# Kernel tuning notes

Measured on AMD Instinct MI355X. Metric: run time of the kernel, lower is better.

Reference implementation:

```python
import jax, jax.numpy as jnp
import numpy as np

B, T, I, H, L = 32768, 30, 4, 64, 32


def _lstm_layer(x, Wih, Whh, bih, bhh):
    """PyTorch-semantics single-layer LSTM, batch_first. Returns (outputs [B,T,H], h_T [B,H])."""
    # Precompute input contribution for all timesteps: [B, T, 4H]
    xg = jnp.einsum('bti,gi->btg', x, Wih) + bih + bhh
    Hh = Whh.shape[1]
    h0 = jnp.zeros((x.shape[0], Hh), x.dtype)

    def step(carry, xg_t):
        h, c = carry
        g = xg_t + h @ Whh.T  # [B, 4H]
        i, f, gg, o = jnp.split(g, 4, axis=-1)  # PyTorch gate order i,f,g,o
        c = jax.nn.sigmoid(f) * c + jax.nn.sigmoid(i) * jnp.tanh(gg)
        h = jax.nn.sigmoid(o) * jnp.tanh(c)
        return (h, c), h

    (hT, _), hs = jax.lax.scan(step, (h0, h0), jnp.swapaxes(xg, 0, 1))
    return jnp.swapaxes(hs, 0, 1), hT


def setup_inputs() -> dict:
    key = jax.random.key(0)
    ks = jax.random.split(key, 20)
    s = 0.1  # weight scale for numerical stability
    inp = {
        'x': jax.random.normal(ks[0], (B, T, I), jnp.float32),
        'enc1_Wih': s * jax.random.normal(ks[1], (4 * H, I), jnp.float32),
        'enc1_Whh': s * jax.random.normal(ks[2], (4 * H, H), jnp.float32),
        'enc1_bih': s * jax.random.normal(ks[3], (4 * H,), jnp.float32),
        'enc1_bhh': s * jax.random.normal(ks[4], (4 * H,), jnp.float32),
        'enc2_Wih': s * jax.random.normal(ks[5], (4 * L, H), jnp.float32),
        'enc2_Whh': s * jax.random.normal(ks[6], (4 * L, L), jnp.float32),
        'enc2_bih': s * jax.random.normal(ks[7], (4 * L,), jnp.float32),
        'enc2_bhh': s * jax.random.normal(ks[8], (4 * L,), jnp.float32),
        'dec1_Wih': s * jax.random.normal(ks[9], (4 * H, L), jnp.float32),
        'dec1_Whh': s * jax.random.normal(ks[10], (4 * H, H), jnp.float32),
        'dec1_bih': s * jax.random.normal(ks[11], (4 * H,), jnp.float32),
        'dec1_bhh': s * jax.random.normal(ks[12], (4 * H,), jnp.float32),
        'dec2_Wih': s * jax.random.normal(ks[13], (4 * I, H), jnp.float32),
        'dec2_Whh': s * jax.random.normal(ks[14], (4 * I, I), jnp.float32),
        'dec2_bih': s * jax.random.normal(ks[15], (4 * I,), jnp.float32),
        'dec2_bhh': s * jax.random.normal(ks[16], (4 * I,), jnp.float32),
    }
    return inp


def reference(x, enc1_Wih, enc1_Whh, enc1_bih, enc1_bhh,
              enc2_Wih, enc2_Whh, enc2_bih, enc2_bhh,
              dec1_Wih, dec1_Whh, dec1_bih, dec1_bhh,
              dec2_Wih, dec2_Whh, dec2_bih, dec2_bhh):
    seq_len = x.shape[1]
    out, _ = _lstm_layer(x, enc1_Wih, enc1_Whh, enc1_bih, enc1_bhh)
    out, h = _lstm_layer(out, enc2_Wih, enc2_Whh, enc2_bih, enc2_bhh)
    latent = jnp.repeat(h[:, None, :], seq_len, axis=1)  # [B, T, L]
    out, _ = _lstm_layer(latent, dec1_Wih, dec1_Whh, dec1_bih, dec1_bhh)
    out, _ = _lstm_layer(out, dec2_Wih, dec2_Whh, dec2_bih, dec2_bhh)
    return out
```

## Files before the change

kernel.cpp:

```cpp
#include <hip/hip_runtime.h>
#include <stdint.h>


typedef unsigned short u16;
typedef unsigned int u32;
typedef __attribute__((ext_vector_type(8))) short bf16x8;
typedef __attribute__((ext_vector_type(4))) float f32x4;
typedef __attribute__((ext_vector_type(4))) u32 u32x4;
typedef __attribute__((ext_vector_type(2))) u32 u32x2;

#define BATCH 32768
#define TT 30
#define IN 4
#define WAVES 8
#define BLOCKT (WAVES * 64)
#define MB 16
#define BPB (WAVES * MB)

#define LOG2E 1.4426950408889634f
#define LOG2E2 2.8853900817779268f

#define O_WHH1 0
#define O_W1C  8192
#define O_WIH2 9216
#define O_WHH2 13312
#define O_WHH3 0
#define O_WIH3 8192
#define O_WIH4 12288
#define O_W4HHF 12800
#define O_B1F 15360
#define O_B2F 15616
#define O_B3F 15744
#define O_B4F 16000
#define O_BUFS 16016
#define PBUF 1088
#define SMEM_WORDS (O_BUFS + WAVES * PBUF)
#define SMEM_BYTES (SMEM_WORDS * 4)

#define WB() __builtin_amdgcn_wave_barrier()
#define MFMA(a, b, c) __builtin_amdgcn_mfma_f32_16x16x32_bf16((a), (b), (c), 0, 0, 0)

__device__ __forceinline__ u16 f2bf(float f) {
    u32 u = __float_as_uint(f);
    u += 0x7fffu + ((u >> 16) & 1u);
    return (u16)(u >> 16);
}
__device__ __forceinline__ float bf2f(u16 v) { return __uint_as_float(((u32)v) << 16); }

__device__ __forceinline__ u32 cvtpk2(float a, float b) {
    u32 d;
    asm("v_cvt_pk_bf16_f32 %0, %1, %2" : "=v"(d) : "v"(a), "v"(b));
    return d;
}

__device__ __forceinline__ float unitH(float yi, float yf, float yg, float yo, float& c) {
    const float ei = __builtin_amdgcn_exp2f(-yi);
    const float ef = __builtin_amdgcn_exp2f(-yf);
    const float eg = __builtin_amdgcn_exp2f(yg);
    const float eo = __builtin_amdgcn_exp2f(-yo);
    const float Z = (1.f + ei) * (1.f + eg);
    const float X = 1.f + ef;
    const float num = fmaf(eg - 1.f, X, c * Z);
    c = num * __builtin_amdgcn_rcpf(X * Z);
    const float ec = __builtin_amdgcn_exp2f(c * LOG2E2);
    return (ec - 1.f) * __builtin_amdgcn_rcpf((1.f + eo) * (1.f + ec));
}

template <int KT, int GS>
__device__ __forceinline__ void stageBh(u16* hi, const float* src, int N, int tid) {
    const int K = KT * 32;
    const int total = N * K;
    for (int idx = tid; idx < total; idx += BLOCKT) {
        const int j = idx & 7;
        const int l = (idx >> 3) & 63;
        const int pr = idx >> 9;
        const int kt = pr & (KT - 1);
        const int nt = pr / KT;
        const int n = (nt << 4) | (l & 15);
        const int k = (kt << 5) + ((l >> 4) << 3) + j;
        const float s = (((n >> GS) & 3) == 2) ? LOG2E2 : LOG2E;
        hi[idx] = f2bf(src[n * K + k] * s);
    }
}

__global__ __launch_bounds__(BLOCKT)
__attribute__((amdgpu_waves_per_eu(2)))
void lstm_ae(
    const float* __restrict__ x,
    const float* __restrict__ w1ih, const float* __restrict__ w1hh,
    const float* __restrict__ b1i, const float* __restrict__ b1h,
    const float* __restrict__ w2ih, const float* __restrict__ w2hh,
    const float* __restrict__ b2i, const float* __restrict__ b2h,
    const float* __restrict__ w3ih, const float* __restrict__ w3hh,
    const float* __restrict__ b3i, const float* __restrict__ b3h,
    const float* __restrict__ w4ih, const float* __restrict__ w4hh,
    const float* __restrict__ b4i, const float* __restrict__ b4h,
    float* __restrict__ out) {
    extern __shared__ float smem[];
    float* W = smem;

    const int tid = threadIdx.x;
    const int wave = tid >> 6, lane = tid & 63;
    const int col = lane & 15, quad = lane >> 4;

    float* pb = smem + O_BUFS + wave * PBUF;
    u16* h1b = (u16*)pb;
    u16* h2b = (u16*)(pb + 512);
    float* gbuf = pb + 768;
    float* bufH4 = pb + 1024;

    const int b0w = blockIdx.x * BPB + wave * MB;
    const int hbase = (col << 3) + ((quad & 1) << 2) + ((quad >> 1) << 7);

    stageBh<2, 6>((u16*)(W + O_WHH1), w1hh, 256, tid);
    stageBh<2, 5>((u16*)(W + O_WIH2), w2ih, 128, tid);
    stageBh<1, 5>((u16*)(W + O_WHH2), w2hh, 128, tid);
    {
        u16* C = (u16*)(W + O_W1C);
        for (int idx = tid; idx < 2048; idx += BLOCKT) {
            const int n = idx >> 3, j = idx & 7;
            const float sc = ((n >> 6) == 2) ? LOG2E2 : LOG2E;
            const float w = w1ih[n * 4 + (j & 3)] * sc;
            C[idx] = (j < 4) ? f2bf(w) : f2bf(w - bf2f(f2bf(w)));
        }
    }
    float* b1f = W + O_B1F;
    float* b2f = W + O_B2F;
    float* b3f = W + O_B3F;
    float* b4f = W + O_B4F;
    for (int i = tid; i < 256; i += BLOCKT)
        b1f[i] = (b1i[i] + b1h[i]) * (((i >> 6) == 2) ? LOG2E2 : LOG2E);
    for (int i = tid; i < 128; i += BLOCKT)
        b2f[i] = (b2i[i] + b2h[i]) * (((i >> 5) == 2) ? LOG2E2 : LOG2E);
    for (int i = tid; i < 256; i += BLOCKT)
        b3f[i] = (b3i[i] + b3h[i]) * (((i >> 6) == 2) ? LOG2E2 : LOG2E);
    for (int i = tid; i < 16; i += BLOCKT)
        b4f[i] = (b4i[i] + b4h[i]) * (((i >> 2) == 2) ? LOG2E2 : LOG2E);
    {
        u32* z = (u32*)pb;
        for (int i = lane; i < 768; i += 64) z[i] = 0u;
    }
    __syncthreads();

    const u16* Whh1hi = (const u16*)(W + O_WHH1);
    const u16* Wih2hi = (const u16*)(W + O_WIH2);
    const u16* Whh2hi = (const u16*)(W + O_WHH2);
    const u16* W1cL = (const u16*)(W + O_W1C) + (col << 3) + ((quad == 1) ? 4 : 0);

    float c1[4][4];
    float c2[2][4];
#pragma unroll
    for (int q = 0; q < 4; ++q)
#pragma unroll
        for (int r = 0; r < 4; ++r) c1[q][r] = 0.f;
#pragma unroll
    for (int q = 0; q < 2; ++q)
#pragma unroll
        for (int r = 0; r < 4; ++r) c2[q][r] = 0.f;

    float4 xcur = *reinterpret_cast<const float4*>(x + ((size_t)(b0w + col) * TT + 0) * IN);

    for (int s = 0; s < TT; ++s) {
        const u32 hi01 = cvtpk2(xcur.x, xcur.y);
        const u32 hi23 = cvtpk2(xcur.z, xcur.w);
        const float r0 = xcur.x - __uint_as_float(hi01 << 16);
        const float r1 = xcur.y - __uint_as_float(hi01 & 0xffff0000u);
        const float r2 = xcur.z - __uint_as_float(hi23 << 16);
        const float r3 = xcur.w - __uint_as_float(hi23 & 0xffff0000u);
        const u32 lo01 = cvtpk2(r0, r1);
        const u32 lo23 = cvtpk2(r2, r3);
        u32x4 xv;
        xv.x = (quad <= 1) ? hi01 : 0u;
        xv.y = (quad <= 1) ? hi23 : 0u;
        xv.z = (quad == 0) ? lo01 : 0u;
        xv.w = (quad == 0) ? lo23 : 0u;
        const bf16x8 a1x = __builtin_bit_cast(bf16x8, xv);
        {
            const int tn = (s + 1 < TT) ? s + 1 : s;
            xcur = *reinterpret_cast<const float4*>(x + ((size_t)(b0w + col) * TT + tn) * IN);
        }
        const bf16x8 a1h0 = *reinterpret_cast<const bf16x8*>(h1b + lane * 8);
        const bf16x8 a1h1 = *reinterpret_cast<const bf16x8*>(h1b + (64 + lane) * 8);
#pragma unroll
        for (int q = 0; q < 4; ++q) {
            f32x4 acc[4];
#pragma unroll
            for (int i = 0; i < 4; ++i) {
                const int nt = i * 4 + q;
                const u32x2 wp = *reinterpret_cast<const u32x2*>(W1cL + nt * 128);
                u32x4 afu;
                afu.x = wp.x; afu.y = wp.y; afu.z = wp.x; afu.w = wp.y;
                const bf16x8 af = __builtin_bit_cast(bf16x8, afu);
                const bf16x8 bh0 = *reinterpret_cast<const bf16x8*>(Whh1hi + ((nt * 2 + 0) * 64 + lane) * 8);
                const bf16x8 bh1 = *reinterpret_cast<const bf16x8*>(Whh1hi + ((nt * 2 + 1) * 64 + lane) * 8);
                f32x4 a = *reinterpret_cast<const f32x4*>(b1f + nt * 16 + (quad << 2));
                a = MFMA(af, a1x, a);
                a = MFMA(bh0, a1h0, a);
                a = MFMA(bh1, a1h1, a);
                acc[i] = a;
            }
            const float h0 = unitH(acc[0][0], acc[1][0], acc[2][0], acc[3][0], c1[q][0]);
            const float h1 = unitH(acc[0][1], acc[1][1], acc[2][1], acc[3][1], c1[q][1]);
            const float h2 = unitH(acc[0][2], acc[1][2], acc[2][2], acc[3][2], c1[q][2]);
            const float h3 = unitH(acc[0][3], acc[1][3], acc[2][3], acc[3][3], c1[q][3]);
            u32x2 wv;
            wv.x = cvtpk2(h0, h1);
            wv.y = cvtpk2(h2, h3);
            *reinterpret_cast<u32x2*>(h1b + hbase + ((q >> 1) << 9) + ((q & 1) << 8)) = wv;
        }
        WB();
        const bf16x8 e1h0 = *reinterpret_cast<const bf16x8*>(h1b + lane * 8);
        const bf16x8 e1h1 = *reinterpret_cast<const bf16x8*>(h1b + (64 + lane) * 8);
        const bf16x8 a2h = *reinterpret_cast<const bf16x8*>(h2b + lane * 8);
        f32x4 acc2[8];
#pragma unroll
        for (int nt = 0; nt < 8; ++nt) {
            const bf16x8 bh0 = *reinterpret_cast<const bf16x8*>(Wih2hi + ((nt * 2 + 0) * 64 + lane) * 8);
            const bf16x8 bh1 = *reinterpret_cast<const bf16x8*>(Wih2hi + ((nt * 2 + 1) * 64 + lane) * 8);
            const bf16x8 ch = *reinterpret_cast<const bf16x8*>(Whh2hi + (nt * 64 + lane) * 8);
            f32x4 a = *reinterpret_cast<const f32x4*>(b2f + nt * 16 + (quad << 2));
            a = MFMA(bh0, e1h0, a);
            a = MFMA(bh1, e1h1, a);
            a = MFMA(ch, a2h, a);
            acc2[nt] = a;
        }
        WB();
#pragma unroll
        for (int q = 0; q < 2; ++q) {
            const float h0 = unitH(acc2[q][0], acc2[2 + q][0], acc2[4 + q][0], acc2[6 + q][0], c2[q][0]);
            const float h1 = unitH(acc2[q][1], acc2[2 + q][1], acc2[4 + q][1], acc2[6 + q][1], c2[q][1]);
            const float h2 = unitH(acc2[q][2], acc2[2 + q][2], acc2[4 + q][2], acc2[6 + q][2], c2[q][2]);
            const float h3 = unitH(acc2[q][3], acc2[2 + q][3], acc2[4 + q][3], acc2[6 + q][3], c2[q][3]);
            u32x2 wv;
            wv.x = cvtpk2(h0, h1);
            wv.y = cvtpk2(h2, h3);
            *reinterpret_cast<u32x2*>(h2b + hbase + (q << 8)) = wv;
        }
        WB();
    }

    __syncthreads();
    stageBh<2, 6>((u16*)(W + O_WHH3), w3hh, 256, tid);
    stageBh<1, 6>((u16*)(W + O_WIH3), w3ih, 256, tid);
    stageBh<2, 2>((u16*)(W + O_WIH4), w4ih, 16, tid);
    for (int i = tid; i < 64; i += BLOCKT)
        W[O_W4HHF + i] = w4hh[i] * ((((i >> 4) & 3) == 2) ? LOG2E2 : LOG2E);

    const bf16x8 aLh = *reinterpret_cast<const bf16x8*>(h2b + lane * 8);
    {
        u32* z = (u32*)pb;
        for (int i = lane; i < 512; i += 64) z[i] = 0u;
        bufH4[lane] = 0.f;
    }
    float c3[4][4];
#pragma unroll
    for (int q = 0; q < 4; ++q)
#pragma unroll
        for (int r = 0; r < 4; ++r) c3[q][r] = 0.f;
    float c4 = 0.f;
    const f32x4 bias4v = *reinterpret_cast<const f32x4*>(b4f + (quad << 2));
    const int u4 = lane & 3, mb = lane >> 2;
    __syncthreads();

    const u16* Whh3hi = (const u16*)(W + O_WHH3);
    const u16* Wih3hi = (const u16*)(W + O_WIH3);
    const u16* Wih4hi = (const u16*)(W + O_WIH4);
    const float* W4hhF = W + O_W4HHF;

    for (int s = 0; s < TT; ++s) {
        const bf16x8 a3h0 = *reinterpret_cast<const bf16x8*>(h1b + lane * 8);
        const bf16x8 a3h1 = *reinterpret_cast<const bf16x8*>(h1b + (64 + lane) * 8);
#pragma unroll
        for (int q = 0; q < 4; ++q) {
            f32x4 acc[4];
#pragma unroll
            for (int i = 0; i < 4; ++i) {
                const int nt = i * 4 + q;
                const bf16x8 bL = *reinterpret_cast<const bf16x8*>(Wih3hi + (nt * 64 + lane) * 8);
                const bf16x8 bh0 = *reinterpret_cast<const bf16x8*>(Whh3hi + ((nt * 2 + 0) * 64 + lane) * 8);
                const bf16x8 bh1 = *reinterpret_cast<const bf16x8*>(Whh3hi + ((nt * 2 + 1) * 64 + lane) * 8);
                f32x4 a = *reinterpret_cast<const f32x4*>(b3f + nt * 16 + (quad << 2));
                a = MFMA(bL, aLh, a);
                a = MFMA(bh0, a3h0, a);
                a = MFMA(bh1, a3h1, a);
                acc[i] = a;
            }
            const float h0 = unitH(acc[0][0], acc[1][0], acc[2][0], acc[3][0], c3[q][0]);
            const float h1 = unitH(acc[0][1], acc[1][1], acc[2][1], acc[3][1], c3[q][1]);
            const float h2 = unitH(acc[0][2], acc[1][2], acc[2][2], acc[3][2], c3[q][2]);
            const float h3 = unitH(acc[0][3], acc[1][3], acc[2][3], acc[3][3], c3[q][3]);
            u32x2 wv;
            wv.x = cvtpk2(h0, h1);
            wv.y = cvtpk2(h2, h3);
            *reinterpret_cast<u32x2*>(h1b + hbase + ((q >> 1) << 9) + ((q & 1) << 8)) = wv;
        }
        WB();
        const bf16x8 d3h0 = *reinterpret_cast<const bf16x8*>(h1b + lane * 8);
        const bf16x8 d3h1 = *reinterpret_cast<const bf16x8*>(h1b + (64 + lane) * 8);
        f32x4 acc4 = bias4v;
        {
            const float4 hv = *reinterpret_cast<const float4*>(bufH4 + (col << 2));
#pragma unroll
            for (int r = 0; r < 4; ++r) {
                const float4 w4 = *reinterpret_cast<const float4*>(W4hhF + ((quad * 4 + r) << 2));
                float sa = acc4[r];
                sa = fmaf(w4.x, hv.x, sa);
                sa = fmaf(w4.y, hv.y, sa);
                sa = fmaf(w4.z, hv.z, sa);
                sa = fmaf(w4.w, hv.w, sa);
                acc4[r] = sa;
            }
        }
        {
            const bf16x8 bh0 = *reinterpret_cast<const bf16x8*>(Wih4hi + (0 * 64 + lane) * 8);
            const bf16x8 bh1 = *reinterpret_cast<const bf16x8*>(Wih4hi + (1 * 64 + lane) * 8);
            acc4 = MFMA(bh0, d3h0, acc4);
            acc4 = MFMA(bh1, d3h1, acc4);
        }
        WB();
        *reinterpret_cast<f32x4*>(gbuf + (col << 4) + (quad << 2)) = acc4;
        WB();
        {
            const float yi = gbuf[mb * 16 + u4];
            const float yf = gbuf[mb * 16 + 4 + u4];
            const float yg = gbuf[mb * 16 + 8 + u4];
            const float yo = gbuf[mb * 16 + 12 + u4];
            const float h = unitH(yi, yf, yg, yo, c4);
            out[((size_t)(b0w + mb) * TT + s) * IN + u4] = h;
            bufH4[mb * 4 + u4] = h;
        }
        WB();
    }
}

extern "C" void kernel_launch(void* const* d_in, const int* in_sizes, int n_in,
                              void* d_out, int out_size, void* d_ws, size_t ws_size,
                              hipStream_t stream) {
    (void)in_sizes; (void)n_in; (void)d_ws; (void)ws_size; (void)out_size;
    hipFuncSetAttribute(reinterpret_cast<const void*>(lstm_ae),
                        hipFuncAttributeMaxDynamicSharedMemorySize, SMEM_BYTES);
    const float* xi = (const float*)d_in[0];
    const float* w1ih = (const float*)d_in[1];
    const float* w1hh = (const float*)d_in[2];
    const float* b1i = (const float*)d_in[3];
    const float* b1h = (const float*)d_in[4];
    const float* w2ih = (const float*)d_in[5];
    const float* w2hh = (const float*)d_in[6];
    const float* b2i = (const float*)d_in[7];
    const float* b2h = (const float*)d_in[8];
    const float* w3ih = (const float*)d_in[9];
    const float* w3hh = (const float*)d_in[10];
    const float* b3i = (const float*)d_in[11];
    const float* b3h = (const float*)d_in[12];
    const float* w4ih = (const float*)d_in[13];
    const float* w4hh = (const float*)d_in[14];
    const float* b4i = (const float*)d_in[15];
    const float* b4h = (const float*)d_in[16];
    float* out = (float*)d_out;

    lstm_ae<<<dim3(BATCH / BPB), dim3(BLOCKT), SMEM_BYTES, stream>>>(
        xi, w1ih, w1hh, b1i, b1h, w2ih, w2hh, b2i, b2h,
        w3ih, w3hh, b3i, b3h, w4ih, w4hh, b4i, b4h, out);
}
```

Baseline: 311.3 us.

## Software-pipeline stacked LSTM layers with double-buffered hidden state

Restructures the encoder and decoder time loops so the next step of layer 1 is computed while layer 2 consumes the current step, using a double-buffered h1 in LDS (per-wave buffer grows). This removes several wave barriers per step and exposes more independent MFMA and transcendental work for interleaving. Biases and small dec2 weights are also hoisted into registers, which raises register pressure and may lower occupancy.

```diff
diff --git a/kernel.cpp b/kernel.cpp
--- a/kernel.cpp
+++ b/kernel.cpp
@@ -33,7 +33,7 @@
 #define O_B3F 15744
 #define O_B4F 16000
 #define O_BUFS 16016
-#define PBUF 1088
+#define PBUF 1600
 #define SMEM_WORDS (O_BUFS + WAVES * PBUF)
 #define SMEM_BYTES (SMEM_WORDS * 4)
 
@@ -104,10 +104,10 @@
     const int col = lane & 15, quad = lane >> 4;
 
     float* pb = smem + O_BUFS + wave * PBUF;
-    u16* h1b = (u16*)pb;
-    u16* h2b = (u16*)(pb + 512);
-    float* gbuf = pb + 768;
-    float* bufH4 = pb + 1024;
+    u16* h1d = (u16*)pb;
+    u16* h2b = (u16*)(pb + 1024);
+    float* gbuf = pb + 1280;
+    float* bufH4 = pb + 1536;
 
     const int b0w = blockIdx.x * BPB + wave * MB;
     const int hbase = (col << 3) + ((quad & 1) << 2) + ((quad >> 1) << 7);
@@ -138,7 +138,8 @@
         b4f[i] = (b4i[i] + b4h[i]) * (((i >> 2) == 2) ? LOG2E2 : LOG2E);
     {
         u32* z = (u32*)pb;
-        for (int i = lane; i < 768; i += 64) z[i] = 0u;
+        for (int i = lane; i < 256; i += 64) z[1024 + i] = 0u;
+        bufH4[lane] = 0.f;
     }
     __syncthreads();
 
@@ -147,6 +148,11 @@
     const u16* Whh2hi = (const u16*)(W + O_WHH2);
     const u16* W1cL = (const u16*)(W + O_W1C) + (col << 3) + ((quad == 1) ? 4 : 0);
 
+    f32x4 b2r[8];
+#pragma unroll
+    for (int nt = 0; nt < 8; ++nt)
+        b2r[nt] = *reinterpret_cast<const f32x4*>(b2f + nt * 16 + (quad << 2));
+
     float c1[4][4];
     float c2[2][4];
 #pragma unroll
@@ -160,13 +166,18 @@
 
     float4 xcur = *reinterpret_cast<const float4*>(x + ((size_t)(b0w + col) * TT + 0) * IN);
 
-    for (int s = 0; s < TT; ++s) {
-        const u32 hi01 = cvtpk2(xcur.x, xcur.y);
-        const u32 hi23 = cvtpk2(xcur.z, xcur.w);
-        const float r0 = xcur.x - __uint_as_float(hi01 << 16);
-        const float r1 = xcur.y - __uint_as_float(hi01 & 0xffff0000u);
-        const float r2 = xcur.z - __uint_as_float(hi23 << 16);
-        const float r3 = xcur.w - __uint_as_float(hi23 & 0xffff0000u);
+    auto enc1_step = [&](const bf16x8 ah0, const bf16x8 ah1, u16* hnext, int tnext) {
+        const float4 xc = xcur;
+        {
+            const int tn = (tnext + 1 < TT) ? tnext + 1 : tnext;
+            xcur = *reinterpret_cast<const float4*>(x + ((size_t)(b0w + col) * TT + tn) * IN);
+        }
+        const u32 hi01 = cvtpk2(xc.x, xc.y);
+        const u32 hi23 = cvtpk2(xc.z, xc.w);
+        const float r0 = xc.x - __uint_as_float(hi01 << 16);
+        const float r1 = xc.y - __uint_as_float(hi01 & 0xffff0000u);
+        const float r2 = xc.z - __uint_as_float(hi23 << 16);
+        const float r3 = xc.w - __uint_as_float(hi23 & 0xffff0000u);
         const u32 lo01 = cvtpk2(r0, r1);
         const u32 lo23 = cvtpk2(r2, r3);
         u32x4 xv;
@@ -175,12 +186,6 @@
         xv.z = (quad == 0) ? lo01 : 0u;
         xv.w = (quad == 0) ? lo23 : 0u;
         const bf16x8 a1x = __builtin_bit_cast(bf16x8, xv);
-        {
-            const int tn = (s + 1 < TT) ? s + 1 : s;
-            xcur = *reinterpret_cast<const float4*>(x + ((size_t)(b0w + col) * TT + tn) * IN);
-        }
-        const bf16x8 a1h0 = *reinterpret_cast<const bf16x8*>(h1b + lane * 8);
-        const bf16x8 a1h1 = *reinterpret_cast<const bf16x8*>(h1b + (64 + lane) * 8);
 #pragma unroll
         for (int q = 0; q < 4; ++q) {
             f32x4 acc[4];
@@ -195,8 +200,8 @@
                 const bf16x8 bh1 = *reinterpret_cast<const bf16x8*>(Whh1hi + ((nt * 2 + 1) * 64 + lane) * 8);
                 f32x4 a = *reinterpret_cast<const f32x4*>(b1f + nt * 16 + (quad << 2));
                 a = MFMA(af, a1x, a);
-                a = MFMA(bh0, a1h0, a);
-                a = MFMA(bh1, a1h1, a);
+                a = MFMA(bh0, ah0, a);
+                a = MFMA(bh1, ah1, a);
                 acc[i] = a;
             }
             const float h0 = unitH(acc[0][0], acc[1][0], acc[2][0], acc[3][0], c1[q][0]);
@@ -206,11 +211,18 @@
             u32x2 wv;
             wv.x = cvtpk2(h0, h1);
             wv.y = cvtpk2(h2, h3);
-            *reinterpret_cast<u32x2*>(h1b + hbase + ((q >> 1) << 9) + ((q & 1) << 8)) = wv;
-        }
-        WB();
-        const bf16x8 e1h0 = *reinterpret_cast<const bf16x8*>(h1b + lane * 8);
-        const bf16x8 e1h1 = *reinterpret_cast<const bf16x8*>(h1b + (64 + lane) * 8);
+            *reinterpret_cast<u32x2*>(hnext + hbase + ((q >> 1) << 9) + ((q & 1) << 8)) = wv;
+        }
+    };
+
+    {
+        const bf16x8 z8 = {};
+        enc1_step(z8, z8, h1d, 0);
+    }
+    for (int t = 0; t < TT - 1; ++t) {
+        const u16* hcur = h1d + ((t & 1) << 10);
+        const bf16x8 ah0 = *reinterpret_cast<const bf16x8*>(hcur + lane * 8);
+        const bf16x8 ah1 = *reinterpret_cast<const bf16x8*>(hcur + (64 + lane) * 8);
         const bf16x8 a2h = *reinterpret_cast<const bf16x8*>(h2b + lane * 8);
         f32x4 acc2[8];
 #pragma unroll
@@ -218,13 +230,13 @@
             const bf16x8 bh0 = *reinterpret_cast<const bf16x8*>(Wih2hi + ((nt * 2 + 0) * 64 + lane) * 8);
             const bf16x8 bh1 = *reinterpret_cast<const bf16x8*>(Wih2hi + ((nt * 2 + 1) * 64 + lane) * 8);
             const bf16x8 ch = *reinterpret_cast<const bf16x8*>(Whh2hi + (nt * 64 + lane) * 8);
-            f32x4 a = *reinterpret_cast<const f32x4*>(b2f + nt * 16 + (quad << 2));
-            a = MFMA(bh0, e1h0, a);
-            a = MFMA(bh1, e1h1, a);
+            f32x4 a = b2r[nt];
+            a = MFMA(bh0, ah0, a);
+            a = MFMA(bh1, ah1, a);
             a = MFMA(ch, a2h, a);
             acc2[nt] = a;
         }
-        WB();
+        enc1_step(ah0, ah1, h1d + (((t + 1) & 1) << 10), t + 1);
 #pragma unroll
         for (int q = 0; q < 2; ++q) {
             const float h0 = unitH(acc2[q][0], acc2[2 + q][0], acc2[4 + q][0], acc2[6 + q][0], c2[q][0]);
@@ -236,7 +248,35 @@
             wv.y = cvtpk2(h2, h3);
             *reinterpret_cast<u32x2*>(h2b + hbase + (q << 8)) = wv;
         }
-        WB();
+    }
+    {
+        const u16* hcur = h1d + (((TT - 1) & 1) << 10);
+        const bf16x8 ah0 = *reinterpret_cast<const bf16x8*>(hcur + lane * 8);
+        const bf16x8 ah1 = *reinterpret_cast<const bf16x8*>(hcur + (64 + lane) * 8);
+        const bf16x8 a2h = *reinterpret_cast<const bf16x8*>(h2b + lane * 8);
+        f32x4 acc2[8];
+#pragma unroll
+        for (int nt = 0; nt < 8; ++nt) {
+            const bf16x8 bh0 = *reinterpret_cast<const bf16x8*>(Wih2hi + ((nt * 2 + 0) * 64 + lane) * 8);
+            const bf16x8 bh1 = *reinterpret_cast<const bf16x8*>(Wih2hi + ((nt * 2 + 1) * 64 + lane) * 8);
+            const bf16x8 ch = *reinterpret_cast<const bf16x8*>(Whh2hi + (nt * 64 + lane) * 8);
+            f32x4 a = b2r[nt];
+            a = MFMA(bh0, ah0, a);
+            a = MFMA(bh1, ah1, a);
+            a = MFMA(ch, a2h, a);
+            acc2[nt] = a;
+        }
+#pragma unroll
+        for (int q = 0; q < 2; ++q) {
+            const float h0 = unitH(acc2[q][0], acc2[2 + q][0], acc2[4 + q][0], acc2[6 + q][0], c2[q][0]);
+            const float h1 = unitH(acc2[q][1], acc2[2 + q][1], acc2[4 + q][1], acc2[6 + q][1], c2[q][1]);
+            const float h2 = unitH(acc2[q][2], acc2[2 + q][2], acc2[4 + q][2], acc2[6 + q][2], c2[q][2]);
+            const float h3 = unitH(acc2[q][3], acc2[2 + q][3], acc2[4 + q][3], acc2[6 + q][3], c2[q][3]);
+            u32x2 wv;
+            wv.x = cvtpk2(h0, h1);
+            wv.y = cvtpk2(h2, h3);
+            *reinterpret_cast<u32x2*>(h2b + hbase + (q << 8)) = wv;
+        }
     }
 
     __syncthreads();
@@ -247,29 +287,30 @@
         W[O_W4HHF + i] = w4hh[i] * ((((i >> 4) & 3) == 2) ? LOG2E2 : LOG2E);
 
     const bf16x8 aLh = *reinterpret_cast<const bf16x8*>(h2b + lane * 8);
-    {
-        u32* z = (u32*)pb;
-        for (int i = lane; i < 512; i += 64) z[i] = 0u;
-        bufH4[lane] = 0.f;
-    }
     float c3[4][4];
 #pragma unroll
     for (int q = 0; q < 4; ++q)
 #pragma unroll
         for (int r = 0; r < 4; ++r) c3[q][r] = 0.f;
     float c4 = 0.f;
-    const f32x4 bias4v = *reinterpret_cast<const f32x4*>(b4f + (quad << 2));
     const int u4 = lane & 3, mb = lane >> 2;
     __syncthreads();
 
     const u16* Whh3hi = (const u16*)(W + O_WHH3);
     const u16* Wih3hi = (const u16*)(W + O_WIH3);
-    const u16* Wih4hi = (const u16*)(W + O_WIH4);
-    const float* W4hhF = W + O_W4HHF;
-
-    for (int s = 0; s < TT; ++s) {
-        const bf16x8 a3h0 = *reinterpret_cast<const bf16x8*>(h1b + lane * 8);
-        const bf16x8 a3h1 = *reinterpret_cast<const bf16x8*>(h1b + (64 + lane) * 8);
+    f32x4 b3r[16];
+#pragma unroll
+    for (int nt = 0; nt < 16; ++nt)
+        b3r[nt] = *reinterpret_cast<const f32x4*>(b3f + nt * 16 + (quad << 2));
+    const f32x4 bias4v = *reinterpret_cast<const f32x4*>(b4f + (quad << 2));
+    const bf16x8 w4f0 = *reinterpret_cast<const bf16x8*>((const u16*)(W + O_WIH4) + (0 * 64 + lane) * 8);
+    const bf16x8 w4f1 = *reinterpret_cast<const bf16x8*>((const u16*)(W + O_WIH4) + (1 * 64 + lane) * 8);
+    float4 w4r[4];
+#pragma unroll
+    for (int r = 0; r < 4; ++r)
+        w4r[r] = *reinterpret_cast<const float4*>(W + O_W4HHF + ((quad * 4 + r) << 2));
+
+    auto dec1_step = [&](const bf16x8 ah0, const bf16x8 ah1, u16* hnext) {
 #pragma unroll
         for (int q = 0; q < 4; ++q) {
             f32x4 acc[4];
@@ -279,10 +320,9 @@
                 const bf16x8 bL = *reinterpret_cast<const bf16x8*>(Wih3hi + (nt * 64 + lane) * 8);
                 const bf16x8 bh0 = *reinterpret_cast<const bf16x8*>(Whh3hi + ((nt * 2 + 0) * 64 + lane) * 8);
                 const bf16x8 bh1 = *reinterpret_cast<const bf16x8*>(Whh3hi + ((nt * 2 + 1) * 64 + lane) * 8);
-                f32x4 a = *reinterpret_cast<const f32x4*>(b3f + nt * 16 + (quad << 2));
-                a = MFMA(bL, aLh, a);
-                a = MFMA(bh0, a3h0, a);
-                a = MFMA(bh1, a3h1, a);
+                f32x4 a = MFMA(bL, aLh, b3r[nt]);
+                a = MFMA(bh0, ah0, a);
+                a = MFMA(bh1, ah1, a);
                 acc[i] = a;
             }
             const float h0 = unitH(acc[0][0], acc[1][0], acc[2][0], acc[3][0], c3[q][0]);
@@ -292,31 +332,34 @@
             u32x2 wv;
             wv.x = cvtpk2(h0, h1);
             wv.y = cvtpk2(h2, h3);
-            *reinterpret_cast<u32x2*>(h1b + hbase + ((q >> 1) << 9) + ((q & 1) << 8)) = wv;
-        }
-        WB();
-        const bf16x8 d3h0 = *reinterpret_cast<const bf16x8*>(h1b + lane * 8);
-        const bf16x8 d3h1 = *reinterpret_cast<const bf16x8*>(h1b + (64 + lane) * 8);
+            *reinterpret_cast<u32x2*>(hnext + hbase + ((q >> 1) << 9) + ((q & 1) << 8)) = wv;
+        }
+    };
+
+    {
+        const bf16x8 z8 = {};
+        dec1_step(z8, z8, h1d);
+    }
+    for (int t = 0; t < TT - 1; ++t) {
+        const u16* hcur = h1d + ((t & 1) << 10);
+        const bf16x8 ah0 = *reinterpret_cast<const bf16x8*>(hcur + lane * 8);
+        const bf16x8 ah1 = *reinterpret_cast<const bf16x8*>(hcur + (64 + lane) * 8);
         f32x4 acc4 = bias4v;
         {
             const float4 hv = *reinterpret_cast<const float4*>(bufH4 + (col << 2));
 #pragma unroll
             for (int r = 0; r < 4; ++r) {
-                const float4 w4 = *reinterpret_cast<const float4*>(W4hhF + ((quad * 4 + r) << 2));
                 float sa = acc4[r];
-                sa = fmaf(w4.x, hv.x, sa);
-                sa = fmaf(w4.y, hv.y, sa);
-                sa = fmaf(w4.z, hv.z, sa);
-                sa = fmaf(w4.w, hv.w, sa);
+                sa = fmaf(w4r[r].x, hv.x, sa);
+                sa = fmaf(w4r[r].y, hv.y, sa);
+                sa = fmaf(w4r[r].z, hv.z, sa);
+                sa = fmaf(w4r[r].w, hv.w, sa);
                 acc4[r] = sa;
             }
         }
-        {
-            const bf16x8 bh0 = *reinterpret_cast<const bf16x8*>(Wih4hi + (0 * 64 + lane) * 8);
-            const bf16x8 bh1 = *reinterpret_cast<const bf16x8*>(Wih4hi + (1 * 64 + lane) * 8);
-            acc4 = MFMA(bh0, d3h0, acc4);
-            acc4 = MFMA(bh1, d3h1, acc4);
-        }
+        acc4 = MFMA(w4f0, ah0, acc4);
+        acc4 = MFMA(w4f1, ah1, acc4);
+        dec1_step(ah0, ah1, h1d + (((t + 1) & 1) << 10));
         WB();
         *reinterpret_cast<f32x4*>(gbuf + (col << 4) + (quad << 2)) = acc4;
         WB();
@@ -326,10 +369,41 @@
             const float yg = gbuf[mb * 16 + 8 + u4];
             const float yo = gbuf[mb * 16 + 12 + u4];
             const float h = unitH(yi, yf, yg, yo, c4);
-            out[((size_t)(b0w + mb) * TT + s) * IN + u4] = h;
+            out[((size_t)(b0w + mb) * TT + t) * IN + u4] = h;
             bufH4[mb * 4 + u4] = h;
         }
+    }
+    {
+        const int t = TT - 1;
+        const u16* hcur = h1d + ((t & 1) << 10);
+        const bf16x8 ah0 = *reinterpret_cast<const bf16x8*>(hcur + lane * 8);
+        const bf16x8 ah1 = *reinterpret_cast<const bf16x8*>(hcur + (64 + lane) * 8);
+        f32x4 acc4 = bias4v;
+        {
+            const float4 hv = *reinterpret_cast<const float4*>(bufH4 + (col << 2));
+#pragma unroll
+            for (int r = 0; r < 4; ++r) {
+                float sa = acc4[r];
+                sa = fmaf(w4r[r].x, hv.x, sa);
+                sa = fmaf(w4r[r].y, hv.y, sa);
+                sa = fmaf(w4r[r].z, hv.z, sa);
+                sa = fmaf(w4r[r].w, hv.w, sa);
+                acc4[r] = sa;
+            }
+        }
+        acc4 = MFMA(w4f0, ah0, acc4);
+        acc4 = MFMA(w4f1, ah1, acc4);
         WB();
+        *reinterpret_cast<f32x4*>(gbuf + (col << 4) + (quad << 2)) = acc4;
+        WB();
+        {
+            const float yi = gbuf[mb * 16 + u4];
+            const float yf = gbuf[mb * 16 + 4 + u4];
+            const float yg = gbuf[mb * 16 + 8 + u4];
+            const float yo = gbuf[mb * 16 + 12 + u4];
+            const float h = unitH(yi, yf, yg, yo, c4);
+            out[((size_t)(b0w + mb) * TT + t) * IN + u4] = h;
+        }
     }
 }
 
```

Result: faster. 299.2 us (-3.9%).

## Split each batch tile across wave pairs and software-pipeline stacked LSTM layers

Applied to the files above, without the earlier changes.

Each 16-row batch tile is now shared by two waves, each computing half of the hidden units, and they exchange state through LDS with block-wide barriers. Layer 2 of step t is interleaved with layer 1 of step t+1, and dec2 with dec1, to shorten the serial chain. The layer-1 bias is folded into the input MFMA through a constant-one column, and the layer-1 input weights are kept in registers. Rows per block are halved and waves_per_eu is raised to 4. This buys more parallelism at the cost of __syncthreads per timestep and tighter register limits.

```diff
diff --git a/kernel.cpp b/kernel.cpp
--- a/kernel.cpp
+++ b/kernel.cpp
@@ -15,26 +15,26 @@
 #define WAVES 8
 #define BLOCKT (WAVES * 64)
 #define MB 16
-#define BPB (WAVES * MB)
+#define NGRP 4
+#define BPB (NGRP * MB)
 
 #define LOG2E 1.4426950408889634f
 #define LOG2E2 2.8853900817779268f
 
 #define O_WHH1 0
 #define O_W1C  8192
-#define O_WIH2 9216
-#define O_WHH2 13312
+#define O_WIH2 10240
+#define O_WHH2 14336
 #define O_WHH3 0
 #define O_WIH3 8192
 #define O_WIH4 12288
 #define O_W4HHF 12800
-#define O_B1F 15360
-#define O_B2F 15616
-#define O_B3F 15744
-#define O_B4F 16000
-#define O_BUFS 16016
-#define PBUF 1088
-#define SMEM_WORDS (O_BUFS + WAVES * PBUF)
+#define O_B2F 16384
+#define O_B3F 16512
+#define O_B4F 16768
+#define O_BUFS 16784
+#define PBUF 832
+#define SMEM_WORDS (O_BUFS + NGRP * PBUF)
 #define SMEM_BYTES (SMEM_WORDS * 4)
 
 #define WB() __builtin_amdgcn_wave_barrier()
@@ -84,7 +84,7 @@
 }
 
 __global__ __launch_bounds__(BLOCKT)
-__attribute__((amdgpu_waves_per_eu(2)))
+__attribute__((amdgpu_waves_per_eu(4)))
 void lstm_ae(
     const float* __restrict__ x,
     const float* __restrict__ w1ih, const float* __restrict__ w1hh,
@@ -101,15 +101,17 @@
 
     const int tid = threadIdx.x;
     const int wave = tid >> 6, lane = tid & 63;
+    const int wg = wave >> 1, wh = wave & 1;
     const int col = lane & 15, quad = lane >> 4;
-
-    float* pb = smem + O_BUFS + wave * PBUF;
+    const int q0 = wh << 1;
+
+    float* pb = smem + O_BUFS + wg * PBUF;
     u16* h1b = (u16*)pb;
     u16* h2b = (u16*)(pb + 512);
-    float* gbuf = pb + 768;
-    float* bufH4 = pb + 1024;
-
-    const int b0w = blockIdx.x * BPB + wave * MB;
+    float* gbuf = pb + 512;
+    float* bufH4 = pb + 768;
+
+    const int b0w = blockIdx.x * BPB + wg * MB;
     const int hbase = (col << 3) + ((quad & 1) << 2) + ((quad >> 1) << 7);
 
     stageBh<2, 6>((u16*)(W + O_WHH1), w1hh, 256, tid);
@@ -117,19 +119,27 @@
     stageBh<1, 5>((u16*)(W + O_WHH2), w2hh, 128, tid);
     {
         u16* C = (u16*)(W + O_W1C);
-        for (int idx = tid; idx < 2048; idx += BLOCKT) {
-            const int n = idx >> 3, j = idx & 7;
+        for (int idx = tid; idx < 256 * 16; idx += BLOCKT) {
+            const int n = idx >> 4, j = idx & 15;
             const float sc = ((n >> 6) == 2) ? LOG2E2 : LOG2E;
-            const float w = w1ih[n * 4 + (j & 3)] * sc;
-            C[idx] = (j < 4) ? f2bf(w) : f2bf(w - bf2f(f2bf(w)));
-        }
-    }
-    float* b1f = W + O_B1F;
+            u16 v = 0;
+            if (j < 4) {
+                v = f2bf(w1ih[n * 4 + j] * sc);
+            } else if (j < 8) {
+                const float w = w1ih[n * 4 + (j - 4)] * sc;
+                v = f2bf(w - bf2f(f2bf(w)));
+            } else if (j == 8) {
+                v = f2bf((b1i[n] + b1h[n]) * sc);
+            } else if (j == 9) {
+                const float b = (b1i[n] + b1h[n]) * sc;
+                v = f2bf(b - bf2f(f2bf(b)));
+            }
+            C[idx] = v;
+        }
+    }
     float* b2f = W + O_B2F;
     float* b3f = W + O_B3F;
     float* b4f = W + O_B4F;
-    for (int i = tid; i < 256; i += BLOCKT)
-        b1f[i] = (b1i[i] + b1h[i]) * (((i >> 6) == 2) ? LOG2E2 : LOG2E);
     for (int i = tid; i < 128; i += BLOCKT)
         b2f[i] = (b2i[i] + b2h[i]) * (((i >> 5) == 2) ? LOG2E2 : LOG2E);
     for (int i = tid; i < 256; i += BLOCKT)
@@ -138,127 +148,162 @@
         b4f[i] = (b4i[i] + b4h[i]) * (((i >> 2) == 2) ? LOG2E2 : LOG2E);
     {
         u32* z = (u32*)pb;
-        for (int i = lane; i < 768; i += 64) z[i] = 0u;
+        if (wh == 0) {
+            for (int i = lane; i < 256; i += 64) z[512 + i] = 0u;
+        } else {
+            bufH4[lane] = 0.f;
+        }
     }
     __syncthreads();
 
     const u16* Whh1hi = (const u16*)(W + O_WHH1);
     const u16* Wih2hi = (const u16*)(W + O_WIH2);
     const u16* Whh2hi = (const u16*)(W + O_WHH2);
-    const u16* W1cL = (const u16*)(W + O_W1C) + (col << 3) + ((quad == 1) ? 4 : 0);
-
-    float c1[4][4];
-    float c2[2][4];
-#pragma unroll
-    for (int q = 0; q < 4; ++q)
-#pragma unroll
-        for (int r = 0; r < 4; ++r) c1[q][r] = 0.f;
-#pragma unroll
-    for (int q = 0; q < 2; ++q)
-#pragma unroll
-        for (int r = 0; r < 4; ++r) c2[q][r] = 0.f;
-
+
+    bf16x8 w1a[2][4];
+    {
+        const u16* Cx = (const u16*)(W + O_W1C);
+#pragma unroll
+        for (int ql = 0; ql < 2; ++ql)
+#pragma unroll
+            for (int i = 0; i < 4; ++i) {
+                const int nt = i * 4 + q0 + ql;
+                const u16* row = Cx + (((nt << 4) | col) << 4);
+                u32x4 v = {0u, 0u, 0u, 0u};
+                if (quad == 0) {
+                    const u32x2 p = *reinterpret_cast<const u32x2*>(row);
+                    v.x = p.x; v.y = p.y; v.z = p.x; v.w = p.y;
+                } else if (quad == 1) {
+                    const u32x2 p = *reinterpret_cast<const u32x2*>(row + 4);
+                    v.x = p.x; v.y = p.y; v.z = p.x; v.w = p.y;
+                } else if (quad == 2) {
+                    v.x = *reinterpret_cast<const u32*>(row + 8);
+                }
+                w1a[ql][i] = __builtin_bit_cast(bf16x8, v);
+            }
+    }
+
+    float c1[2][4];
+    float c2v[4];
+#pragma unroll
+    for (int ql = 0; ql < 2; ++ql)
+#pragma unroll
+        for (int r = 0; r < 4; ++r) c1[ql][r] = 0.f;
+#pragma unroll
+    for (int r = 0; r < 4; ++r) c2v[r] = 0.f;
+
+    const f32x4 zf = {0.f, 0.f, 0.f, 0.f};
     float4 xcur = *reinterpret_cast<const float4*>(x + ((size_t)(b0w + col) * TT + 0) * IN);
 
-    for (int s = 0; s < TT; ++s) {
-        const u32 hi01 = cvtpk2(xcur.x, xcur.y);
-        const u32 hi23 = cvtpk2(xcur.z, xcur.w);
-        const float r0 = xcur.x - __uint_as_float(hi01 << 16);
-        const float r1 = xcur.y - __uint_as_float(hi01 & 0xffff0000u);
-        const float r2 = xcur.z - __uint_as_float(hi23 << 16);
-        const float r3 = xcur.w - __uint_as_float(hi23 & 0xffff0000u);
+    auto buildX = [&](const float4 xc) -> bf16x8 {
+        const u32 hi01 = cvtpk2(xc.x, xc.y);
+        const u32 hi23 = cvtpk2(xc.z, xc.w);
+        const float r0 = xc.x - __uint_as_float(hi01 << 16);
+        const float r1 = xc.y - __uint_as_float(hi01 & 0xffff0000u);
+        const float r2 = xc.z - __uint_as_float(hi23 << 16);
+        const float r3 = xc.w - __uint_as_float(hi23 & 0xffff0000u);
         const u32 lo01 = cvtpk2(r0, r1);
         const u32 lo23 = cvtpk2(r2, r3);
         u32x4 xv;
-        xv.x = (quad <= 1) ? hi01 : 0u;
+        xv.x = (quad <= 1) ? hi01 : ((quad == 2) ? 0x3F803F80u : 0u);
         xv.y = (quad <= 1) ? hi23 : 0u;
         xv.z = (quad == 0) ? lo01 : 0u;
         xv.w = (quad == 0) ? lo23 : 0u;
-        const bf16x8 a1x = __builtin_bit_cast(bf16x8, xv);
-        {
-            const int tn = (s + 1 < TT) ? s + 1 : s;
-            xcur = *reinterpret_cast<const float4*>(x + ((size_t)(b0w + col) * TT + tn) * IN);
-        }
-        const bf16x8 a1h0 = *reinterpret_cast<const bf16x8*>(h1b + lane * 8);
-        const bf16x8 a1h1 = *reinterpret_cast<const bf16x8*>(h1b + (64 + lane) * 8);
-#pragma unroll
-        for (int q = 0; q < 4; ++q) {
+        return __builtin_bit_cast(bf16x8, xv);
+    };
+
+    auto enc1_half = [&](const bf16x8 a1x, const bf16x8 ah0, const bf16x8 ah1) {
+#pragma unroll
+        for (int ql = 0; ql < 2; ++ql) {
             f32x4 acc[4];
 #pragma unroll
             for (int i = 0; i < 4; ++i) {
-                const int nt = i * 4 + q;
-                const u32x2 wp = *reinterpret_cast<const u32x2*>(W1cL + nt * 128);
-                u32x4 afu;
-                afu.x = wp.x; afu.y = wp.y; afu.z = wp.x; afu.w = wp.y;
-                const bf16x8 af = __builtin_bit_cast(bf16x8, afu);
+                const int nt = i * 4 + q0 + ql;
                 const bf16x8 bh0 = *reinterpret_cast<const bf16x8*>(Whh1hi + ((nt * 2 + 0) * 64 + lane) * 8);
                 const bf16x8 bh1 = *reinterpret_cast<const bf16x8*>(Whh1hi + ((nt * 2 + 1) * 64 + lane) * 8);
-                f32x4 a = *reinterpret_cast<const f32x4*>(b1f + nt * 16 + (quad << 2));
-                a = MFMA(af, a1x, a);
-                a = MFMA(bh0, a1h0, a);
-                a = MFMA(bh1, a1h1, a);
+                f32x4 a = MFMA(w1a[ql][i], a1x, zf);
+                a = MFMA(bh0, ah0, a);
+                a = MFMA(bh1, ah1, a);
                 acc[i] = a;
             }
-            const float h0 = unitH(acc[0][0], acc[1][0], acc[2][0], acc[3][0], c1[q][0]);
-            const float h1 = unitH(acc[0][1], acc[1][1], acc[2][1], acc[3][1], c1[q][1]);
-            const float h2 = unitH(acc[0][2], acc[1][2], acc[2][2], acc[3][2], c1[q][2]);
-            const float h3 = unitH(acc[0][3], acc[1][3], acc[2][3], acc[3][3], c1[q][3]);
+            const float h0 = unitH(acc[0][0], acc[1][0], acc[2][0], acc[3][0], c1[ql][0]);
+            const float h1 = unitH(acc[0][1], acc[1][1], acc[2][1], acc[3][1], c1[ql][1]);
+            const float h2 = unitH(acc[0][2], acc[1][2], acc[2][2], acc[3][2], c1[ql][2]);
+            const float h3 = unitH(acc[0][3], acc[1][3], acc[2][3], acc[3][3], c1[ql][3]);
             u32x2 wv;
             wv.x = cvtpk2(h0, h1);
             wv.y = cvtpk2(h2, h3);
-            *reinterpret_cast<u32x2*>(h1b + hbase + ((q >> 1) << 9) + ((q & 1) << 8)) = wv;
-        }
-        WB();
-        const bf16x8 e1h0 = *reinterpret_cast<const bf16x8*>(h1b + lane * 8);
-        const bf16x8 e1h1 = *reinterpret_cast<const bf16x8*>(h1b + (64 + lane) * 8);
-        const bf16x8 a2h = *reinterpret_cast<const bf16x8*>(h2b + lane * 8);
-        f32x4 acc2[8];
-#pragma unroll
-        for (int nt = 0; nt < 8; ++nt) {
+            *reinterpret_cast<u32x2*>(h1b + hbase + (wh << 9) + (ql << 8)) = wv;
+        }
+    };
+    auto enc2_half = [&](const bf16x8 ah0, const bf16x8 ah1, const bf16x8 a2h) {
+        f32x4 g4[4];
+#pragma unroll
+        for (int g = 0; g < 4; ++g) {
+            const int nt = g * 2 + wh;
             const bf16x8 bh0 = *reinterpret_cast<const bf16x8*>(Wih2hi + ((nt * 2 + 0) * 64 + lane) * 8);
             const bf16x8 bh1 = *reinterpret_cast<const bf16x8*>(Wih2hi + ((nt * 2 + 1) * 64 + lane) * 8);
             const bf16x8 ch = *reinterpret_cast<const bf16x8*>(Whh2hi + (nt * 64 + lane) * 8);
             f32x4 a = *reinterpret_cast<const f32x4*>(b2f + nt * 16 + (quad << 2));
-            a = MFMA(bh0, e1h0, a);
-            a = MFMA(bh1, e1h1, a);
+            a = MFMA(bh0, ah0, a);
+            a = MFMA(bh1, ah1, a);
             a = MFMA(ch, a2h, a);
-            acc2[nt] = a;
-        }
-        WB();
-#pragma unroll
-        for (int q = 0; q < 2; ++q) {
-            const float h0 = unitH(acc2[q][0], acc2[2 + q][0], acc2[4 + q][0], acc2[6 + q][0], c2[q][0]);
-            const float h1 = unitH(acc2[q][1], acc2[2 + q][1], acc2[4 + q][1], acc2[6 + q][1], c2[q][1]);
-            const float h2 = unitH(acc2[q][2], acc2[2 + q][2], acc2[4 + q][2], acc2[6 + q][2], c2[q][2]);
-            const float h3 = unitH(acc2[q][3], acc2[2 + q][3], acc2[4 + q][3], acc2[6 + q][3], c2[q][3]);
-            u32x2 wv;
-            wv.x = cvtpk2(h0, h1);
-            wv.y = cvtpk2(h2, h3);
-            *reinterpret_cast<u32x2*>(h2b + hbase + (q << 8)) = wv;
-        }
-        WB();
-    }
-
+            g4[g] = a;
+        }
+        const float h0 = unitH(g4[0][0], g4[1][0], g4[2][0], g4[3][0], c2v[0]);
+        const float h1 = unitH(g4[0][1], g4[1][1], g4[2][1], g4[3][1], c2v[1]);
+        const float h2 = unitH(g4[0][2], g4[1][2], g4[2][2], g4[3][2], c2v[2]);
+        const float h3 = unitH(g4[0][3], g4[1][3], g4[2][3], g4[3][3], c2v[3]);
+        u32x2 wv;
+        wv.x = cvtpk2(h0, h1);
+        wv.y = cvtpk2(h2, h3);
+        *reinterpret_cast<u32x2*>(h2b + hbase + (wh << 8)) = wv;
+    };
+
+    {
+        const bf16x8 z8 = {};
+        const bf16x8 a1x = buildX(xcur);
+        xcur = *reinterpret_cast<const float4*>(x + ((size_t)(b0w + col) * TT + 1) * IN);
+        enc1_half(a1x, z8, z8);
+    }
     __syncthreads();
+
+    for (int t = 0; t < TT - 1; ++t) {
+        const bf16x8 ah0 = *reinterpret_cast<const bf16x8*>(h1b + lane * 8);
+        const bf16x8 ah1 = *reinterpret_cast<const bf16x8*>(h1b + (64 + lane) * 8);
+        const bf16x8 a2h = *reinterpret_cast<const bf16x8*>(h2b + lane * 8);
+        __syncthreads();
+        enc2_half(ah0, ah1, a2h);
+        const bf16x8 a1x = buildX(xcur);
+        {
+            const int tn = (t + 2 < TT) ? t + 2 : TT - 1;
+            xcur = *reinterpret_cast<const float4*>(x + ((size_t)(b0w + col) * TT + tn) * IN);
+        }
+        enc1_half(a1x, ah0, ah1);
+        __syncthreads();
+    }
+    {
+        const bf16x8 ah0 = *reinterpret_cast<const bf16x8*>(h1b + lane * 8);
+        const bf16x8 ah1 = *reinterpret_cast<const bf16x8*>(h1b + (64 + lane) * 8);
+        const bf16x8 a2h = *reinterpret_cast<const bf16x8*>(h2b + lane * 8);
+        __syncthreads();
+        enc2_half(ah0, ah1, a2h);
+    }
+    __syncthreads();
+    const bf16x8 aLh = *reinterpret_cast<const bf16x8*>(h2b + lane * 8);
+
     stageBh<2, 6>((u16*)(W + O_WHH3), w3hh, 256, tid);
     stageBh<1, 6>((u16*)(W + O_WIH3), w3ih, 256, tid);
     stageBh<2, 2>((u16*)(W + O_WIH4), w4ih, 16, tid);
     for (int i = tid; i < 64; i += BLOCKT)
         W[O_W4HHF + i] = w4hh[i] * ((((i >> 4) & 3) == 2) ? LOG2E2 : LOG2E);
 
-    const bf16x8 aLh = *reinterpret_cast<const bf16x8*>(h2b + lane * 8);
-    {
-        u32* z = (u32*)pb;
-        for (int i = lane; i < 512; i += 64) z[i] = 0u;
-        bufH4[lane] = 0.f;
-    }
-    float c3[4][4];
-#pragma unroll
-    for (int q = 0; q < 4; ++q)
-#pragma unroll
-        for (int r = 0; r < 4; ++r) c3[q][r] = 0.f;
+    float c3[2][4];
+#pragma unroll
+    for (int ql = 0; ql < 2; ++ql)
+#pragma unroll
+        for (int r = 0; r < 4; ++r) c3[ql][r] = 0.f;
     float c4 = 0.f;
-    const f32x4 bias4v = *reinterpret_cast<const f32x4*>(b4f + (quad << 2));
     const int u4 = lane & 3, mb = lane >> 2;
     __syncthreads();
 
@@ -266,70 +311,85 @@
     const u16* Wih3hi = (const u16*)(W + O_WIH3);
     const u16* Wih4hi = (const u16*)(W + O_WIH4);
     const float* W4hhF = W + O_W4HHF;
-
-    for (int s = 0; s < TT; ++s) {
-        const bf16x8 a3h0 = *reinterpret_cast<const bf16x8*>(h1b + lane * 8);
-        const bf16x8 a3h1 = *reinterpret_cast<const bf16x8*>(h1b + (64 + lane) * 8);
-#pragma unroll
-        for (int q = 0; q < 4; ++q) {
+    const f32x4 bias4v = *reinterpret_cast<const f32x4*>(b4f + (quad << 2));
+
+    auto dec1_half = [&](const bf16x8 ah0, const bf16x8 ah1) {
+#pragma unroll
+        for (int ql = 0; ql < 2; ++ql) {
             f32x4 acc[4];
 #pragma unroll
             for (int i = 0; i < 4; ++i) {
-                const int nt = i * 4 + q;
+                const int nt = i * 4 + q0 + ql;
                 const bf16x8 bL = *reinterpret_cast<const bf16x8*>(Wih3hi + (nt * 64 + lane) * 8);
                 const bf16x8 bh0 = *reinterpret_cast<const bf16x8*>(Whh3hi + ((nt * 2 + 0) * 64 + lane) * 8);
                 const bf16x8 bh1 = *reinterpret_cast<const bf16x8*>(Whh3hi + ((nt * 2 + 1) * 64 + lane) * 8);
                 f32x4 a = *reinterpret_cast<const f32x4*>(b3f + nt * 16 + (quad << 2));
                 a = MFMA(bL, aLh, a);
-                a = MFMA(bh0, a3h0, a);
-                a = MFMA(bh1, a3h1, a);
+                a = MFMA(bh0, ah0, a);
+                a = MFMA(bh1, ah1, a);
                 acc[i] = a;
             }
-            const float h0 = unitH(acc[0][0], acc[1][0], acc[2][0], acc[3][0], c3[q][0]);
-            const float h1 = unitH(acc[0][1], acc[1][1], acc[2][1], acc[3][1], c3[q][1]);
-            const float h2 = unitH(acc[0][2], acc[1][2], acc[2][2], acc[3][2], c3[q][2]);
-            const float h3 = unitH(acc[0][3], acc[1][3], acc[2][3], acc[3][3], c3[q][3]);
+            const float h0 = unitH(acc[0][0], acc[1][0], acc[2][0], acc[3][0], c3[ql][0]);
+            const float h1 = unitH(acc[0][1], acc[1][1], acc[2][1], acc[3][1], c3[ql][1]);
+            const float h2 = unitH(acc[0][2], acc[1][2], acc[2][2], acc[3][2], c3[ql][2]);
+            const float h3 = unitH(acc[0][3], acc[1][3], acc[2][3], acc[3][3], c3[ql][3]);
             u32x2 wv;
             wv.x = cvtpk2(h0, h1);
             wv.y = cvtpk2(h2, h3);
-            *reinterpret_cast<u32x2*>(h1b + hbase + ((q >> 1) << 9) + ((q & 1) << 8)) = wv;
-        }
-        WB();
-        const bf16x8 d3h0 = *reinterpret_cast<const bf16x8*>(h1b + lane * 8);
-        const bf16x8 d3h1 = *reinterpret_cast<const bf16x8*>(h1b + (64 + lane) * 8);
+            *reinterpret_cast<u32x2*>(h1b + hbase + (wh << 9) + (ql << 8)) = wv;
+        }
+    };
+    auto dec2_step = [&](const bf16x8 ah0, const bf16x8 ah1, const float4 hv, int t) {
         f32x4 acc4 = bias4v;
-        {
-            const float4 hv = *reinterpret_cast<const float4*>(bufH4 + (col << 2));
-#pragma unroll
-            for (int r = 0; r < 4; ++r) {
-                const float4 w4 = *reinterpret_cast<const float4*>(W4hhF + ((quad * 4 + r) << 2));
-                float sa = acc4[r];
-                sa = fmaf(w4.x, hv.x, sa);
-                sa = fmaf(w4.y, hv.y, sa);
-                sa = fmaf(w4.z, hv.z, sa);
-                sa = fmaf(w4.w, hv.w, sa);
-                acc4[r] = sa;
-            }
-        }
-        {
-            const bf16x8 bh0 = *reinterpret_cast<const bf16x8*>(Wih4hi + (0 * 64 + lane) * 8);
-            const bf16x8 bh1 = *reinterpret_cast<const bf16x8*>(Wih4hi + (1 * 64 + lane) * 8);
-            acc4 = MFMA(bh0, d3h0, acc4);
-            acc4 = MFMA(bh1, d3h1, acc4);
-        }
+#pragma unroll
+        for (int r = 0; r < 4; ++r) {
+            const float4 w4 = *reinterpret_cast<const float4*>(W4hhF + ((quad * 4 + r) << 2));
+            float sa = acc4[r];
+            sa = fmaf(w4.x, hv.x, sa);
+            sa = fmaf(w4.y, hv.y, sa);
+            sa = fmaf(w4.z, hv.z, sa);
+            sa = fmaf(w4.w, hv.w, sa);
+            acc4[r] = sa;
+        }
+        const bf16x8 w4f0 = *reinterpret_cast<const bf16x8*>(Wih4hi + (0 * 64 + lane) * 8);
+        const bf16x8 w4f1 = *reinterpret_cast<const bf16x8*>(Wih4hi + (1 * 64 + lane) * 8);
+        acc4 = MFMA(w4f0, ah0, acc4);
+        acc4 = MFMA(w4f1, ah1, acc4);
         WB();
         *reinterpret_cast<f32x4*>(gbuf + (col << 4) + (quad << 2)) = acc4;
         WB();
-        {
-            const float yi = gbuf[mb * 16 + u4];
-            const float yf = gbuf[mb * 16 + 4 + u4];
-            const float yg = gbuf[mb * 16 + 8 + u4];
-            const float yo = gbuf[mb * 16 + 12 + u4];
-            const float h = unitH(yi, yf, yg, yo, c4);
-            out[((size_t)(b0w + mb) * TT + s) * IN + u4] = h;
-            bufH4[mb * 4 + u4] = h;
-        }
-        WB();
+        const float yi = gbuf[mb * 16 + u4];
+        const float yf = gbuf[mb * 16 + 4 + u4];
+        const float yg = gbuf[mb * 16 + 8 + u4];
+        const float yo = gbuf[mb * 16 + 12 + u4];
+        const float h = unitH(yi, yf, yg, yo, c4);
+        out[((size_t)(b0w + mb) * TT + t) * IN + u4] = h;
+        bufH4[mb * 4 + u4] = h;
+    };
+
+    {
+        const bf16x8 z8 = {};
+        dec1_half(z8, z8);
+    }
+    __syncthreads();
+
+    for (int t = 0; t < TT - 1; ++t) {
+        const bf16x8 ah0 = *reinterpret_cast<const bf16x8*>(h1b + lane * 8);
+        const bf16x8 ah1 = *reinterpret_cast<const bf16x8*>(h1b + (64 + lane) * 8);
+        float4 hv = {0.f, 0.f, 0.f, 0.f};
+        if (wh) hv = *reinterpret_cast<const float4*>(bufH4 + (col << 2));
+        __syncthreads();
+        if (wh) dec2_step(ah0, ah1, hv, t);
+        dec1_half(ah0, ah1);
+        __syncthreads();
+    }
+    {
+        const bf16x8 ah0 = *reinterpret_cast<const bf16x8*>(h1b + lane * 8);
+        const bf16x8 ah1 = *reinterpret_cast<const bf16x8*>(h1b + (64 + lane) * 8);
+        if (wh) {
+            const float4 hv = *reinterpret_cast<const float4*>(bufH4 + (col << 2));
+            dec2_step(ah0, ah1, hv, TT - 1);
+        }
     }
 }
 
```

New measurement: 308.1 us. Within noise of the previous version (-1.0%).
